# Kernel tuning notes

Hardware: AMD Instinct MI355X
Metric: run time of the kernel (lower is better)

## Reference

```python
import jax, jax.numpy as jnp
import numpy as np
import math

D_MODEL = 1024
NHEAD = 16
FACTOR = 5


def setup_inputs() -> dict:
    key = jax.random.key(0)
    kq, kk, kv = jax.random.split(key, 3)
    B, L = 4, 2048
    Q = jax.random.normal(kq, (B, L, D_MODEL), dtype=jnp.float32)
    K = jax.random.normal(kk, (B, L, D_MODEL), dtype=jnp.float32)
    V = jax.random.normal(kv, (B, L, D_MODEL), dtype=jnp.float32)
    return {"Q": Q, "K": K, "V": V}


def reference(Q, K, V):
    B, q_len, _ = Q.shape
    k_len = K.shape[1]
    head_dim = D_MODEL // NHEAD
    scale = 1.0 / math.sqrt(head_dim)

    # [B, H, L, Dh]
    Qh = Q.reshape(B, q_len, NHEAD, head_dim).transpose(0, 2, 1, 3)
    Kh = K.reshape(B, k_len, NHEAD, head_dim).transpose(0, 2, 1, 3)
    Vh = V.reshape(B, k_len, NHEAD, head_dim).transpose(0, 2, 1, 3)

    # Dense scores for KL-based query selection
    scores = jnp.einsum('bhqd,bhkd->bhqk', Qh, Kh) * scale
    logp = jax.nn.log_softmax(scores, axis=-1)
    probs = jnp.exp(logp)
    # KL(p || uniform) = sum p * (log p + log k_len)
    kl_div = jnp.sum(probs * (logp + jnp.log(jnp.float32(k_len))), axis=-1)  # [B,H,Q]

    top_u = min(int(FACTOR * math.log(q_len)), q_len)
    _, indices = jax.lax.top_k(kl_div, top_u)  # [B,H,U]

    # Gather selected queries
    Q_sparse = jnp.take_along_axis(Qh, indices[..., None], axis=2)  # [B,H,U,Dh]
    scores_sparse = jnp.einsum('bhud,bhkd->bhuk', Q_sparse, Kh) * scale
    attn_weights = jax.nn.softmax(scores_sparse, axis=-1)  # dropout p=0 (eval)
    output_sparse = jnp.einsum('bhuk,bhkd->bhud', attn_weights, Vh)

    # Scatter back into full-length output (non-selected queries are zero)
    b_idx = jnp.arange(B)[:, None, None]
    h_idx = jnp.arange(NHEAD)[None, :, None]
    output_full = jnp.zeros_like(Qh).at[b_idx, h_idx, indices].set(output_sparse)

    output = output_full.transpose(0, 2, 1, 3).reshape(B, q_len, D_MODEL)
    return output, attn_weights
```

## Files before the change

### kernel.cpp

```cpp
#include <hip/hip_runtime.h>
#include <math.h>

#define LQ 2048
#define DM 1024
#define NH 16
#define DH 64
#define UU 38
#define NBH 64
#define SCALE 0.125f

typedef _Float16 f16x8 __attribute__((ext_vector_type(8)));
typedef float f32x4 __attribute__((ext_vector_type(4)));
typedef float f32x2 __attribute__((ext_vector_type(2)));

#if __has_builtin(__builtin_amdgcn_exp2f)
#define EXP2F(x) __builtin_amdgcn_exp2f(x)
#else
#define EXP2F(x) exp2f(x)
#endif

#define GL2LDS16(gp, lp)                                           \
  __builtin_amdgcn_global_load_lds(                                \
      (const __attribute__((address_space(1))) void*)(gp),         \
      (__attribute__((address_space(3))) void*)(lp), 16, 0, 0)

#define F_OFF_SEL   4194304
#define F_OFF_L3    4204032
#define F_OFF_MASK  4213760
#define F_OFF_LPART 4344832
#define F_OFF_KSP   7146496
#define F_NEED      40700928ull

__global__ __launch_bounds__(256) void ksplit_kernel(const float* __restrict__ K,
                                                     _Float16* __restrict__ ksp) {
  int idx = blockIdx.x * 256 + threadIdx.x;
  int p = idx & 7;
  int k = (idx >> 3) & 63;
  int kc = (idx >> 9) & 31;
  int bh = idx >> 14;
  int b = bh >> 4, h = bh & 15;
  const float* src = K + ((size_t)(b * LQ + kc * 64 + k)) * DM + h * DH + (p ^ (k & 7)) * 8;
  float4 x0 = *(const float4*)src;
  float4 x1 = *(const float4*)(src + 4);
  f16x8 hi, lo;
#define KCV(i, xx) { float x_ = (xx); _Float16 hh = (_Float16)x_; hi[i] = hh; lo[i] = (_Float16)(x_ - (float)hh); }
  KCV(0, x0.x) KCV(1, x0.y) KCV(2, x0.z) KCV(3, x0.w)
  KCV(4, x1.x) KCV(5, x1.y) KCV(6, x1.z) KCV(7, x1.w)
#undef KCV
  _Float16* base = ksp + ((size_t)(bh * 32 + kc)) * 8192;
  *(f16x8*)(base + k * 64 + p * 8) = hi;
  *(f16x8*)(base + 4096 + k * 64 + p * 8) = lo;
}

__global__ __launch_bounds__(256) void kl_mfma2(const float* __restrict__ Q,
                                                const _Float16* __restrict__ ksp,
                                                double* __restrict__ lt) {
  int bh = blockIdx.x & 63;
  int qc = (blockIdx.x >> 6) & 15;
  int sp = blockIdx.x >> 10;
  int b = bh >> 4, h = bh & 15;
  int t = threadIdx.x;
  int lane = t & 63, w = t >> 6;
  int quad = lane >> 4, l15 = lane & 15;

  __shared__ __align__(16) _Float16 kbuf[8192];

  f16x8 ahi[2][2], alo[2][2];
  {
    const float* qrow = Q + ((size_t)(b * LQ + qc * 128)) * DM + h * DH;
#pragma unroll
    for (int qt = 0; qt < 2; ++qt)
#pragma unroll
      for (int c = 0; c < 2; ++c) {
        const float* p = qrow + (size_t)(w * 32 + qt * 16 + l15) * DM + c * 32 + quad * 8;
        float4 x0 = *(const float4*)p;
        float4 x1 = *(const float4*)(p + 4);
        f16x8 hi, lo;
#define QCV(i, xx) { float x_ = (xx); _Float16 hh = (_Float16)x_; hi[i] = hh; lo[i] = (_Float16)(x_ - (float)hh); }
        QCV(0, x0.x) QCV(1, x0.y) QCV(2, x0.z) QCV(3, x0.w)
        QCV(4, x1.x) QCV(5, x1.y) QCV(6, x1.z) QCV(7, x1.w)
#undef QCV
        ahi[qt][c] = hi;
        alo[qt][c] = lo;
      }
  }

  int bsw0 = quad ^ (l15 & 7);
  int bsw1 = (quad + 4) ^ (l15 & 7);
  const float C1 = 0.18033688011112042f;

  double l64[2][4], t64[2][4];
#pragma unroll
  for (int qt = 0; qt < 2; ++qt)
#pragma unroll
    for (int r = 0; r < 4; ++r) { l64[qt][r] = 0.0; t64[qt][r] = 0.0; }

  const _Float16* khiA = kbuf;
  const _Float16* kloA = kbuf + 2048;
  const _Float16* khiB = kbuf + 4096;
  const _Float16* kloB = kbuf + 6144;

  const char* gp = (const char*)(ksp + ((size_t)(bh * 32 + sp * 16)) * 8192) + t * 16;
  char* ldsA = (char*)kbuf + w * 1024;
  char* ldsB = (char*)kbuf + 8192 + w * 1024;

#define KLSTEP(KHI, KLO)                                                        \
  _Pragma("unroll")                                                             \
  for (int kt = 0; kt < 2; ++kt) {                                              \
    int key = kt * 16 + l15;                                                    \
    f16x8 bhi0 = *(const f16x8*)((KHI) + key * 64 + bsw0 * 8);                  \
    f16x8 bhi1 = *(const f16x8*)((KHI) + key * 64 + bsw1 * 8);                  \
    f16x8 blo0 = *(const f16x8*)((KLO) + key * 64 + bsw0 * 8);                  \
    f16x8 blo1 = *(const f16x8*)((KLO) + key * 64 + bsw1 * 8);                  \
    _Pragma("unroll")                                                           \
    for (int qt = 0; qt < 2; ++qt) {                                            \
      f32x4 cacc = {0.f, 0.f, 0.f, 0.f};                                        \
      cacc = __builtin_amdgcn_mfma_f32_16x16x32_f16(alo[qt][0], bhi0, cacc, 0, 0, 0); \
      cacc = __builtin_amdgcn_mfma_f32_16x16x32_f16(alo[qt][1], bhi1, cacc, 0, 0, 0); \
      cacc = __builtin_amdgcn_mfma_f32_16x16x32_f16(ahi[qt][0], blo0, cacc, 0, 0, 0); \
      cacc = __builtin_amdgcn_mfma_f32_16x16x32_f16(ahi[qt][1], blo1, cacc, 0, 0, 0); \
      cacc = __builtin_amdgcn_mfma_f32_16x16x32_f16(ahi[qt][0], bhi0, cacc, 0, 0, 0); \
      cacc = __builtin_amdgcn_mfma_f32_16x16x32_f16(ahi[qt][1], bhi1, cacc, 0, 0, 0); \
      _Pragma("unroll")                                                         \
      for (int rp = 0; rp < 2; ++rp) {                                          \
        f32x2 rr = { cacc[2 * rp], cacc[2 * rp + 1] };                          \
        f32x2 sc = rr * C1;                                   \
        f32x2 e  = { EXP2F(sc[0]), EXP2F(sc[1]) };                              \
        l32[qt][rp] += e;                                     \
        t32[qt][rp] += rr * e;                                \
      }                                                                         \
    }                                                                           \
  }

  GL2LDS16(gp, ldsA);
  GL2LDS16(gp + 8192, ldsA + 4096);
  __syncthreads();

  for (int j = 0; j < 16; ++j) {
    GL2LDS16(gp + 4096, ldsB);
    GL2LDS16(gp + 12288, ldsB + 4096);

    f32x2 l32[2][2], t32[2][2];
#pragma unroll
    for (int qt = 0; qt < 2; ++qt)
#pragma unroll
      for (int rp = 0; rp < 2; ++rp) {
        l32[qt][rp] = (f32x2){0.f, 0.f};
        t32[qt][rp] = (f32x2){0.f, 0.f};
      }

    KLSTEP(khiA, kloA)
    __syncthreads();

    if (j < 15) {
      gp += 16384;
      GL2LDS16(gp, ldsA);
      GL2LDS16(gp + 8192, ldsA + 4096);
    }

    KLSTEP(khiB, kloB)

#pragma unroll
    for (int qt = 0; qt < 2; ++qt)
#pragma unroll
      for (int rp = 0; rp < 2; ++rp)
#pragma unroll
        for (int c = 0; c < 2; ++c) {
          l64[qt][rp * 2 + c] += (double)l32[qt][rp][c];
          t64[qt][rp * 2 + c] += (double)t32[qt][rp][c];
        }
    __syncthreads();
  }
#undef KLSTEP

#pragma unroll
  for (int qt = 0; qt < 2; ++qt)
#pragma unroll
    for (int r = 0; r < 4; ++r) {
      double lv = l64[qt][r], tv = t64[qt][r];
#pragma unroll
      for (int m = 1; m < 16; m <<= 1) {
        lv += __shfl_xor(lv, m);
        tv += __shfl_xor(tv, m);
      }
      if (l15 == 0) {
        int qg = qc * 128 + w * 32 + qt * 16 + quad * 4 + r;
        double* dst = lt + ((size_t)(sp * 64 + bh) * LQ + qg) * 2;
        dst[0] = lv;
        dst[1] = tv;
      }
    }
}

__global__ __launch_bounds__(64) void topk2(const double* __restrict__ lt,
                                            int* __restrict__ idxout,
                                            signed char* __restrict__ selmask,
                                            float* __restrict__ l3out) {
  int bh = blockIdx.x;
  int lane = threadIdx.x;
  __shared__ double vals[LQ];
  __shared__ float lsh[LQ];
  const double logL = 7.624618986159398;

  double v1 = -INFINITY, v2 = -INFINITY, v3 = -INFINITY;
  int i1 = LQ, i2 = LQ, i3 = LQ;

  for (int j = 0; j < 32; ++j) {
    int i = j * 64 + lane;
    const double* p0 = lt + ((size_t)bh * LQ + i) * 2;
    const double* p1 = lt + ((size_t)(64 + bh) * LQ + i) * 2;
    double l = p0[0] + p1[0];
    double tt = p0[1] + p1[1];
    double v = 0.125 * (tt / l) - log(l) + logL;
    vals[i] = v;
    lsh[i] = (float)l;
    selmask[bh * LQ + i] = -1;
    if (v > v1)      { v3 = v2; i3 = i2; v2 = v1; i2 = i1; v1 = v; i1 = i; }
    else if (v > v2) { v3 = v2; i3 = i2; v2 = v;  i2 = i; }
    else if (v > v3) { v3 = v;  i3 = i; }
  }

  for (int u = 0; u < UU; ++u) {
    if (i1 == LQ) {
      v1 = v2 = v3 = -INFINITY;
      i1 = i2 = i3 = LQ;
      for (int j = 0; j < 32; ++j) {
        int i = j * 64 + lane;
        double v = vals[i];
        if (v > v1)      { v3 = v2; i3 = i2; v2 = v1; i2 = i1; v1 = v; i1 = i; }
        else if (v > v2) { v3 = v2; i3 = i2; v2 = v;  i2 = i; }
        else if (v > v3) { v3 = v;  i3 = i; }
      }
    }

    double gv = v1;
    int gi = i1;
#pragma unroll
    for (int m = 1; m < 64; m <<= 1) {
      double ov = __shfl_xor(gv, m);
      int oi = __shfl_xor(gi, m);
      if (ov > gv || (ov == gv && oi < gi)) { gv = ov; gi = oi; }
    }
    if (lane == 0) {
      idxout[bh * UU + u] = gi;
      selmask[bh * LQ + gi] = (signed char)u;
    }
    if ((gi & 63) == lane) {
      l3out[bh * UU + u] = lsh[gi];
      vals[gi] = -INFINITY;
      v1 = v2; i1 = i2;
      v2 = v3; i2 = i3;
      v3 = -INFINITY; i3 = LQ;
    }
  }
}

__global__ __launch_bounds__(256) void attn_w_pv(const float* __restrict__ Q,
                                                 const _Float16* __restrict__ ksp,
                                                 const int* __restrict__ sel,
                                                 const float* __restrict__ l3,
                                                 const float* __restrict__ V,
                                                 float* __restrict__ wout,
                                                 float* __restrict__ kspf) {
  int bh = blockIdx.x >> 4;
  int ks = blockIdx.x & 15;
  int b = bh >> 4, h = bh & 15;
  int t = threadIdx.x;
  int lane = t & 63, w = t >> 6;
  int quad = lane >> 4, l15 = lane & 15;

  __shared__ __align__(16) _Float16 kbuf[8192];
  __shared__ float els[48 * 132];
  __shared__ int sidx[UU];
  __shared__ float l3i[48];

  if (t < UU) sidx[t] = sel[bh * UU + t];
  if (t < 48) l3i[t] = (t < UU) ? 1.f / l3[bh * UU + t] : 0.f;
  __syncthreads();

  f16x8 ahi[3][2], alo[3][2];
#pragma unroll
  for (int qt = 0; qt < 3; ++qt) {
    int u = qt * 16 + l15;
    if (u > 37) u = 37;
    const float* qrow = Q + ((size_t)(b * LQ + sidx[u])) * DM + h * DH;
#pragma unroll
    for (int c = 0; c < 2; ++c) {
      const float* p = qrow + c * 32 + quad * 8;
      float4 x0 = *(const float4*)p;
      float4 x1 = *(const float4*)(p + 4);
      f16x8 hi, lo;
#define QCV(i, xx) { float x_ = (xx); _Float16 hh = (_Float16)x_; hi[i] = hh; lo[i] = (_Float16)(x_ - (float)hh); }
      QCV(0, x0.x) QCV(1, x0.y) QCV(2, x0.z) QCV(3, x0.w)
      QCV(4, x1.x) QCV(5, x1.y) QCV(6, x1.z) QCV(7, x1.w)
#undef QCV
      ahi[qt][c] = hi;
      alo[qt][c] = lo;
    }
  }

  int bsw0 = quad ^ (l15 & 7);
  int bsw1 = (quad + 4) ^ (l15 & 7);
  const float C1 = 0.18033688011112042f;
  const char* gch = (const char*)(ksp + ((size_t)(bh * 32 + ks * 2)) * 8192);
  _Float16* khi = kbuf;
  _Float16* klo = kbuf + 4096;

  for (int chunk = 0; chunk < 2; ++chunk) {
    __syncthreads();
    {
      const char* gs = gch + (size_t)chunk * 16384 + (size_t)t * 16;
      char* ls = (char*)kbuf + (size_t)(w * 64) * 16;
#pragma unroll
      for (int i = 0; i < 4; ++i)
        GL2LDS16(gs + i * 4096, ls + i * 4096);
    }
    __syncthreads();
    int key = w * 16 + l15;
    f16x8 bhi0 = *(const f16x8*)(khi + key * 64 + bsw0 * 8);
    f16x8 bhi1 = *(const f16x8*)(khi + key * 64 + bsw1 * 8);
    f16x8 blo0 = *(const f16x8*)(klo + key * 64 + bsw0 * 8);
    f16x8 blo1 = *(const f16x8*)(klo + key * 64 + bsw1 * 8);
#pragma unroll
    for (int qt = 0; qt < 3; ++qt) {
      f32x4 cacc = {0.f, 0.f, 0.f, 0.f};
      cacc = __builtin_amdgcn_mfma_f32_16x16x32_f16(alo[qt][0], bhi0, cacc, 0, 0, 0);
      cacc = __builtin_amdgcn_mfma_f32_16x16x32_f16(alo[qt][1], bhi1, cacc, 0, 0, 0);
      cacc = __builtin_amdgcn_mfma_f32_16x16x32_f16(ahi[qt][0], blo0, cacc, 0, 0, 0);
      cacc = __builtin_amdgcn_mfma_f32_16x16x32_f16(ahi[qt][1], blo1, cacc, 0, 0, 0);
      cacc = __builtin_amdgcn_mfma_f32_16x16x32_f16(ahi[qt][0], bhi0, cacc, 0, 0, 0);
      cacc = __builtin_amdgcn_mfma_f32_16x16x32_f16(ahi[qt][1], bhi1, cacc, 0, 0, 0);
#pragma unroll
      for (int r = 0; r < 4; ++r) {
        int row = qt * 16 + quad * 4 + r;
        float e = EXP2F(cacc[r] * C1) * l3i[row];
        els[row * 132 + chunk * 64 + w * 16 + l15] = e;
      }
    }
  }
  __syncthreads();

  for (int i = t; i < UU * 128; i += 256) {
    int u = i >> 7, k = i & 127;
    wout[((size_t)(bh * UU + u)) * LQ + ks * 128 + k] = els[u * 132 + k];
  }

  int d = t & 63, ug = t >> 6;
  const float* vbase = V + ((size_t)(b * LQ + ks * 128)) * DM + h * DH + d;
  float o[10];
#pragma unroll
  for (int p = 0; p < 10; ++p) o[p] = 0.f;

  for (int j4 = 0; j4 < 128; j4 += 4) {
    float v0 = vbase[(size_t)(j4 + 0) * DM];
    float v1 = vbase[(size_t)(j4 + 1) * DM];
    float v2 = vbase[(size_t)(j4 + 2) * DM];
    float v3 = vbase[(size_t)(j4 + 3) * DM];
#pragma unroll
    for (int p = 0; p < 10; ++p) {
      float4 pw = *(const float4*)(els + (ug + 4 * p) * 132 + j4);
      o[p] = fmaf(pw.x, v0, o[p]);
      o[p] = fmaf(pw.y, v1, o[p]);
      o[p] = fmaf(pw.z, v2, o[p]);
      o[p] = fmaf(pw.w, v3, o[p]);
    }
  }

  float* oslice = kspf + (size_t)(bh * 32 + ks * 2) * 4096;
#pragma unroll
  for (int p = 0; p < 10; ++p) {
    int u = ug + 4 * p;
    if (u < UU) oslice[u * 64 + d] = o[p];
  }
}

__global__ __launch_bounds__(256) void writeout_kernel(const signed char* __restrict__ selmask,
                                                       const float* __restrict__ kspf,
                                                       float* __restrict__ out) {
  int i2 = blockIdx.x * 256 + threadIdx.x;
  int d = i2 & 63;
  int h = (i2 >> 6) & 15;
  int q = (i2 >> 10) & 2047;
  int b = i2 >> 21;
  int bh = b * 16 + h;
  int u = selmask[bh * LQ + q];
  float val = 0.f;
  if (u >= 0) {
    const float* base = kspf + (size_t)(bh * 32) * 4096 + u * 64 + d;
    float s = 0.f;
#pragma unroll
    for (int p = 0; p < 16; ++p)
      s += base[(size_t)(p * 2) * 4096];
    val = s;
  }
  out[i2] = val;
}

extern "C" void kernel_launch(void* const* d_in, const int* in_sizes, int n_in,
                              void* d_out, int out_size, void* d_ws, size_t ws_size,
                              hipStream_t stream) {
  (void)in_sizes; (void)n_in;
  if (ws_size < F_NEED) return;
  const float* Q = (const float*)d_in[0];
  const float* K = (const float*)d_in[1];
  const float* V = (const float*)d_in[2];
  float* out = (float*)d_out;
  float* wout = out + (size_t)4 * LQ * DM;
  char* ws = (char*)d_ws;

  double* lt = (double*)ws;
  int* sel = (int*)(ws + F_OFF_SEL);
  float* l3 = (float*)(ws + F_OFF_L3);
  signed char* mask = (signed char*)(ws + F_OFF_MASK);
  _Float16* ksp = (_Float16*)(ws + F_OFF_KSP);
  float* kspf = (float*)(ws + F_OFF_KSP);

  ksplit_kernel<<<4096, 256, 0, stream>>>(K, ksp);
  kl_mfma2<<<2048, 256, 0, stream>>>(Q, ksp, lt);
  topk2<<<NBH, 64, 0, stream>>>(lt, sel, mask, l3);
  attn_w_pv<<<NBH * 16, 256, 0, stream>>>(Q, ksp, sel, l3, V, wout, kspf);
  writeout_kernel<<<(4 * LQ * DM) / 256, 256, 0, stream>>>(mask, kspf, out);
}
```

Baseline: 345.0 us.

## Fuse output zeroing into ksplit and scatter PV results with atomics

Removes the separate writeout kernel and the selection mask. The ksplit kernel now also zero-fills the output buffer, and attn_w_pv atomically adds each key-split partial (scaled by the inverse normaliser) straight into the selected query rows. It also wraps the MFMA block in the KL kernel with s_setprio to raise wave priority. This saves one full output pass and the partial-sum workspace traffic, at the cost of float atomics whose summation order is nondeterministic.

Result: no change. 341.2 us (-1.1%).

```diff
diff --git a/kernel.cpp b/kernel.cpp
--- a/kernel.cpp
+++ b/kernel.cpp
@@ -32,7 +32,8 @@
 #define F_NEED      40700928ull
 
 __global__ __launch_bounds__(256) void ksplit_kernel(const float* __restrict__ K,
-                                                     _Float16* __restrict__ ksp) {
+                                                     _Float16* __restrict__ ksp,
+                                                     float* __restrict__ outz) {
   int idx = blockIdx.x * 256 + threadIdx.x;
   int p = idx & 7;
   int k = (idx >> 3) & 63;
@@ -50,6 +51,10 @@
   _Float16* base = ksp + ((size_t)(bh * 32 + kc)) * 8192;
   *(f16x8*)(base + k * 64 + p * 8) = hi;
   *(f16x8*)(base + 4096 + k * 64 + p * 8) = lo;
+
+  float4 z = {0.f, 0.f, 0.f, 0.f};
+  *(float4*)(outz + (size_t)idx * 8) = z;
+  *(float4*)(outz + (size_t)idx * 8 + 4) = z;
 }
 
 __global__ __launch_bounds__(256) void kl_mfma2(const float* __restrict__ Q,
@@ -115,12 +120,14 @@
     _Pragma("unroll")                                                           \
     for (int qt = 0; qt < 2; ++qt) {                                            \
       f32x4 cacc = {0.f, 0.f, 0.f, 0.f};                                        \
+      __builtin_amdgcn_s_setprio(1);                                            \
       cacc = __builtin_amdgcn_mfma_f32_16x16x32_f16(alo[qt][0], bhi0, cacc, 0, 0, 0); \
       cacc = __builtin_amdgcn_mfma_f32_16x16x32_f16(alo[qt][1], bhi1, cacc, 0, 0, 0); \
       cacc = __builtin_amdgcn_mfma_f32_16x16x32_f16(ahi[qt][0], blo0, cacc, 0, 0, 0); \
       cacc = __builtin_amdgcn_mfma_f32_16x16x32_f16(ahi[qt][1], blo1, cacc, 0, 0, 0); \
       cacc = __builtin_amdgcn_mfma_f32_16x16x32_f16(ahi[qt][0], bhi0, cacc, 0, 0, 0); \
       cacc = __builtin_amdgcn_mfma_f32_16x16x32_f16(ahi[qt][1], bhi1, cacc, 0, 0, 0); \
+      __builtin_amdgcn_s_setprio(0);                                            \
       _Pragma("unroll")                                                         \
       for (int rp = 0; rp < 2; ++rp) {                                          \
         f32x2 rr = { cacc[2 * rp], cacc[2 * rp + 1] };                          \
@@ -194,7 +201,6 @@
 
 __global__ __launch_bounds__(64) void topk2(const double* __restrict__ lt,
                                             int* __restrict__ idxout,
-                                            signed char* __restrict__ selmask,
                                             float* __restrict__ l3out) {
   int bh = blockIdx.x;
   int lane = threadIdx.x;
@@ -214,7 +220,6 @@
     double v = 0.125 * (tt / l) - log(l) + logL;
     vals[i] = v;
     lsh[i] = (float)l;
-    selmask[bh * LQ + i] = -1;
     if (v > v1)      { v3 = v2; i3 = i2; v2 = v1; i2 = i1; v1 = v; i1 = i; }
     else if (v > v2) { v3 = v2; i3 = i2; v2 = v;  i2 = i; }
     else if (v > v3) { v3 = v;  i3 = i; }
@@ -241,10 +246,7 @@
       int oi = __shfl_xor(gi, m);
       if (ov > gv || (ov == gv && oi < gi)) { gv = ov; gi = oi; }
     }
-    if (lane == 0) {
-      idxout[bh * UU + u] = gi;
-      selmask[bh * LQ + gi] = (signed char)u;
-    }
+    if (lane == 0) idxout[bh * UU + u] = gi;
     if ((gi & 63) == lane) {
       l3out[bh * UU + u] = lsh[gi];
       vals[gi] = -INFINITY;
@@ -261,7 +263,7 @@
                                                  const float* __restrict__ l3,
                                                  const float* __restrict__ V,
                                                  float* __restrict__ wout,
-                                                 float* __restrict__ kspf) {
+                                                 float* __restrict__ out) {
   int bh = blockIdx.x >> 4;
   int ks = blockIdx.x & 15;
   int b = bh >> 4, h = bh & 15;
@@ -333,8 +335,7 @@
 #pragma unroll
       for (int r = 0; r < 4; ++r) {
         int row = qt * 16 + quad * 4 + r;
-        float e = EXP2F(cacc[r] * C1) * l3i[row];
-        els[row * 132 + chunk * 64 + w * 16 + l15] = e;
+        els[row * 132 + chunk * 64 + w * 16 + l15] = EXP2F(cacc[r] * C1);
       }
     }
   }
@@ -342,7 +343,7 @@
 
   for (int i = t; i < UU * 128; i += 256) {
     int u = i >> 7, k = i & 127;
-    wout[((size_t)(bh * UU + u)) * LQ + ks * 128 + k] = els[u * 132 + k];
+    wout[((size_t)(bh * UU + u)) * LQ + ks * 128 + k] = els[u * 132 + k] * l3i[u];
   }
 
   int d = t & 63, ug = t >> 6;
@@ -366,34 +367,14 @@
     }
   }
 
-  float* oslice = kspf + (size_t)(bh * 32 + ks * 2) * 4096;
 #pragma unroll
   for (int p = 0; p < 10; ++p) {
     int u = ug + 4 * p;
-    if (u < UU) oslice[u * 64 + d] = o[p];
-  }
-}
-
-__global__ __launch_bounds__(256) void writeout_kernel(const signed char* __restrict__ selmask,
-                                                       const float* __restrict__ kspf,
-                                                       float* __restrict__ out) {
-  int i2 = blockIdx.x * 256 + threadIdx.x;
-  int d = i2 & 63;
-  int h = (i2 >> 6) & 15;
-  int q = (i2 >> 10) & 2047;
-  int b = i2 >> 21;
-  int bh = b * 16 + h;
-  int u = selmask[bh * LQ + q];
-  float val = 0.f;
-  if (u >= 0) {
-    const float* base = kspf + (size_t)(bh * 32) * 4096 + u * 64 + d;
-    float s = 0.f;
-#pragma unroll
-    for (int p = 0; p < 16; ++p)
-      s += base[(size_t)(p * 2) * 4096];
-    val = s;
-  }
-  out[i2] = val;
+    if (u < UU) {
+      float* dst = out + ((size_t)(b * LQ + sidx[u])) * DM + h * DH + d;
+      atomicAdd(dst, o[p] * l3i[u]);
+    }
+  }
 }
 
 extern "C" void kernel_launch(void* const* d_in, const int* in_sizes, int n_in,
@@ -411,13 +392,10 @@
   double* lt = (double*)ws;
   int* sel = (int*)(ws + F_OFF_SEL);
   float* l3 = (float*)(ws + F_OFF_L3);
-  signed char* mask = (signed char*)(ws + F_OFF_MASK);
   _Float16* ksp = (_Float16*)(ws + F_OFF_KSP);
-  float* kspf = (float*)(ws + F_OFF_KSP);
-
-  ksplit_kernel<<<4096, 256, 0, stream>>>(K, ksp);
+
+  ksplit_kernel<<<4096, 256, 0, stream>>>(K, ksp, out);
   kl_mfma2<<<2048, 256, 0, stream>>>(Q, ksp, lt);
-  topk2<<<NBH, 64, 0, stream>>>(lt, sel, mask, l3);
-  attn_w_pv<<<NBH * 16, 256, 0, stream>>>(Q, ksp, sel, l3, V, wout, kspf);
-  writeout_kernel<<<(4 * LQ * DM) / 256, 256, 0, stream>>>(mask, kspf, out);
+  topk2<<<NBH, 64, 0, stream>>>(lt, sel, l3);
+  attn_w_pv<<<NBH * 16, 256, 0, stream>>>(Q, ksp, sel, l3, V, wout, out);
 }
```
